# Kernel optimization log

Measured on AMD Instinct MI355X. Metric: run time of the kernel, lower is better.

## Reference

```python
import jax, jax.numpy as jnp
import numpy as np

D_MODEL = 512
N_HEADS = 8
D_K = D_MODEL // N_HEADS


def setup_inputs() -> dict:
    key = jax.random.key(0)
    k1, k2, k3 = jax.random.split(key, 3)
    x = jax.random.normal(k1, (2, 4096, D_MODEL), dtype=jnp.float32)
    # torch Linear weights: [out, in]; we store transposed [in, out] for x @ W
    s_qkv = 1.0 / np.sqrt(D_MODEL)
    W_qkv = jax.random.uniform(k2, (D_MODEL, 3 * D_MODEL), dtype=jnp.float32, minval=-s_qkv, maxval=s_qkv)
    W_out = jax.random.uniform(k3, (D_MODEL, D_MODEL), dtype=jnp.float32, minval=-s_qkv, maxval=s_qkv)
    return {"x": x, "W_qkv": W_qkv, "W_out": W_out}


def reference(x, W_qkv, W_out):
    B, S, _ = x.shape
    qkv = (x @ W_qkv).reshape(B, S, 3, N_HEADS, D_K)
    q, k, v = qkv[:, :, 0], qkv[:, :, 1], qkv[:, :, 2]  # [B,S,H,Dk]
    scale = 1.0 / np.sqrt(D_K).astype(np.float32)
    scores = jnp.einsum('bshd,bthd->bhst', q, k) * scale  # [B,H,S,S]
    attn = jax.nn.softmax(scores, axis=-1)
    out = jnp.einsum('bhst,bthd->bshd', attn, v).reshape(B, S, D_MODEL)
    return out @ W_out
```

## Files before the change

### kernel.cpp

```cpp
#include <hip/hip_runtime.h>
#include <hip/hip_bf16.h>

#define SEQ 4096
#define NB 2
#define DM 512
#define NH 8
#define DK 64

typedef __bf16 bf16;
typedef __bf16 bf16x4 __attribute__((ext_vector_type(4)));
typedef __bf16 bf16x8 __attribute__((ext_vector_type(8)));
typedef float  f32x4 __attribute__((ext_vector_type(4)));

__device__ __forceinline__ f32x4 mfma16(bf16x8 a, bf16x8 b, f32x4 c) {
    return __builtin_amdgcn_mfma_f32_16x16x32_bf16(a, b, c, 0, 0, 0);
}

__device__ __forceinline__ float fexp2(float x) {
    return __builtin_amdgcn_exp2f(x);
}

__device__ __forceinline__ void gload_lds16(const bf16* g, bf16* l) {
    __builtin_amdgcn_global_load_lds(
        (const __attribute__((address_space(1))) void*)g,
        (__attribute__((address_space(3))) void*)l, 16, 0, 0);
}

__device__ __forceinline__ int swzE(int row, int e) {
    return row * 64 + (e ^ ((row & 7) << 3));
}

__device__ __forceinline__ bf16x8 cvt8(const float* __restrict__ p) {
    const float4 v0 = *(const float4*)p;
    const float4 v1 = *(const float4*)(p + 4);
    return (bf16x8){(bf16)v0.x, (bf16)v0.y, (bf16)v0.z, (bf16)v0.w,
                    (bf16)v1.x, (bf16)v1.y, (bf16)v1.z, (bf16)v1.w};
}

__global__ __launch_bounds__(256)
void prep_w2(const float* __restrict__ Wqkv, const float* __restrict__ Wout,
             bf16* __restrict__ Wqh, bf16* __restrict__ Woh) {
    __shared__ float T[64][65];
    const int t = threadIdx.x;
    const int bx = blockIdx.x, by = blockIdx.y;
    const float* W; bf16* D; int N, n0;
    if (by < 24) { W = Wqkv; D = Wqh; N = 3 * DM; n0 = by * 64; }
    else         { W = Wout; D = Woh; N = DM;     n0 = (by - 24) * 64; }
    const int k0 = bx * 64;
    #pragma unroll
    for (int i = 0; i < 4; ++i) {
        int r = i * 16 + (t >> 4);
        int c = (t & 15) * 4;
        float4 v = *(const float4*)&W[(size_t)(k0 + r) * N + n0 + c];
        T[r][c + 0] = v.x; T[r][c + 1] = v.y; T[r][c + 2] = v.z; T[r][c + 3] = v.w;
    }
    __syncthreads();
    #pragma unroll
    for (int i = 0; i < 4; ++i) {
        int n = i * 16 + (t >> 4);
        int c = (t & 15) * 4;
        bf16x4 hv = (bf16x4){(bf16)T[c + 0][n], (bf16)T[c + 1][n],
                             (bf16)T[c + 2][n], (bf16)T[c + 3][n]};
        *(bf16x4*)&D[(size_t)(n0 + n) * DM + k0 + c] = hv;
    }
}

__global__ __launch_bounds__(256, 2)
void gemm_qkv(const float* __restrict__ A, const bf16* __restrict__ Bth,
              bf16* __restrict__ Qout, bf16* __restrict__ Kout,
              bf16* __restrict__ Vout, int M, int N, int K) {
    __shared__ __align__(16) char smem_raw[36864];
    bf16* Ah = (bf16*)smem_raw;
    bf16* Bh = Ah + 128 * 64;

    const int t = threadIdx.x;
    const int lane = t & 63, w = t >> 6;
    const int l15 = lane & 15, g = lane >> 4;
    const int wm = (w >> 1) * 64, wn = (w & 1) * 64;
    const int rowA = blockIdx.y * 128;
    const int colB = blockIdx.x * 128;
    const int sr = t >> 1;
    const int sc = (t & 1) * 32;

    f32x4 acc[4][4] = {};

    for (int k0 = 0; k0 < K; k0 += 64) {
        __syncthreads();
        #pragma unroll
        for (int u = 0; u < 4; ++u) {
            int off = swzE(sr, sc + u * 8);
            *(bf16x8*)&Ah[off] = cvt8(&A[(size_t)(rowA + sr) * K + k0 + sc + u * 8]);
        }
        #pragma unroll
        for (int u = 0; u < 4; ++u) {
            int off = swzE(sr, sc + u * 8);
            *(bf16x8*)&Bh[off] = *(const bf16x8*)&Bth[(size_t)(colB + sr) * K + k0 + sc + u * 8];
        }
        __syncthreads();
        #pragma unroll
        for (int kst = 0; kst < 2; ++kst) {
            bf16x8 ah[4];
            #pragma unroll
            for (int mi = 0; mi < 4; ++mi) {
                int off = swzE(wm + mi * 16 + l15, kst * 32 + g * 8);
                ah[mi] = *(const bf16x8*)&Ah[off];
            }
            #pragma unroll
            for (int ni = 0; ni < 4; ++ni) {
                int off = swzE(wn + ni * 16 + l15, kst * 32 + g * 8);
                bf16x8 bh = *(const bf16x8*)&Bh[off];
                #pragma unroll
                for (int mi = 0; mi < 4; ++mi)
                    acc[mi][ni] = mfma16(ah[mi], bh, acc[mi][ni]);
            }
        }
    }

    const int sec = colB >> 9;
    const float scl = (sec == 0) ? 0.125f * 1.44269504088896f : 1.0f;
    bf16* TB = (bf16*)smem_raw;
    __syncthreads();
    #pragma unroll
    for (int mi = 0; mi < 4; ++mi)
        #pragma unroll
        for (int ni = 0; ni < 4; ++ni)
            #pragma unroll
            for (int r = 0; r < 4; ++r) {
                const int rr = wm + mi * 16 + g * 4 + r;
                const int cr = wn + ni * 16 + l15;
                const float v = acc[mi][ni][r] * scl;
                if (sec < 2) {
                    TB[rr * 136 + cr] = (bf16)v;
                } else {
                    const int kk = rr & 63;
                    const int nn = kk >> 4;
                    const int sl = ((nn & 1) << 5) | (((kk >> 2) & 3) << 3)
                                 | ((nn >> 1) << 2) | (kk & 3);
                    TB[cr * 136 + (rr >> 6) * 64 + sl] = (bf16)v;
                }
            }
    __syncthreads();
    const int b_ = rowA >> 12;
    const int sbase = rowA & 4095;
    #pragma unroll
    for (int pass = 0; pass < 8; ++pass) {
        const int rowi = pass * 16 + (t >> 4);
        const int e8 = (t & 15) * 8;
        bf16x8 v = *(const bf16x8*)&TB[rowi * 136 + e8];
        if (sec < 2) {
            const int ckv = (colB & 511) + e8;
            const int h_ = ckv >> 6, d8 = ckv & 63;
            bf16* dst = (sec == 0) ? Qout : Kout;
            *(bf16x8*)&dst[(((size_t)b_ * NH + h_) * SEQ + sbase + rowi) * DK + d8] = v;
        } else {
            const int cv = (colB - 1024) + rowi;
            const int h_ = cv >> 6, d_ = cv & 63;
            *(bf16x8*)&Vout[(((size_t)b_ * NH + h_) * DK + d_) * SEQ + sbase + e8] = v;
        }
    }
}

__global__ __launch_bounds__(256, 2)
void gemm_out(const bf16* __restrict__ A, const bf16* __restrict__ Bth,
              float* __restrict__ C, int M, int N, int K) {
    __shared__ __align__(16) bf16 Ah[128 * 64], Bh[128 * 64];

    const int t = threadIdx.x;
    const int lane = t & 63, w = t >> 6;
    const int l15 = lane & 15, g = lane >> 4;
    const int wm = (w >> 1) * 64, wn = (w & 1) * 64;
    const int rowA = blockIdx.y * 128;
    const int colB = blockIdx.x * 128;
    const int sr = t >> 1;
    const int sc = (t & 1) * 32;

    f32x4 acc[4][4] = {};

    for (int k0 = 0; k0 < K; k0 += 64) {
        __syncthreads();
        #pragma unroll
        for (int u = 0; u < 4; ++u) {
            int off = swzE(sr, sc + u * 8);
            *(bf16x8*)&Ah[off] = *(const bf16x8*)&A[(size_t)(rowA + sr) * K + k0 + sc + u * 8];
            *(bf16x8*)&Bh[off] = *(const bf16x8*)&Bth[(size_t)(colB + sr) * K + k0 + sc + u * 8];
        }
        __syncthreads();
        #pragma unroll
        for (int kst = 0; kst < 2; ++kst) {
            bf16x8 ah[4];
            #pragma unroll
            for (int mi = 0; mi < 4; ++mi) {
                int off = swzE(wm + mi * 16 + l15, kst * 32 + g * 8);
                ah[mi] = *(const bf16x8*)&Ah[off];
            }
            #pragma unroll
            for (int ni = 0; ni < 4; ++ni) {
                int off = swzE(wn + ni * 16 + l15, kst * 32 + g * 8);
                bf16x8 bh = *(const bf16x8*)&Bh[off];
                #pragma unroll
                for (int mi = 0; mi < 4; ++mi)
                    acc[mi][ni] = mfma16(ah[mi], bh, acc[mi][ni]);
            }
        }
    }
    #pragma unroll
    for (int mi = 0; mi < 4; ++mi)
        #pragma unroll
        for (int ni = 0; ni < 4; ++ni)
            #pragma unroll
            for (int r = 0; r < 4; ++r) {
                int row = rowA + wm + mi * 16 + g * 4 + r;
                int col = colB + wn + ni * 16 + l15;
                C[(size_t)row * N + col] = acc[mi][ni][r];
            }
}

__global__ __launch_bounds__(512)
void flash_mfma(const bf16* __restrict__ Qh,
                const bf16* __restrict__ Kh, const bf16* __restrict__ Vth,
                bf16* __restrict__ att) {
    extern __shared__ bf16 smem[];
    bf16* KhS = smem;
    bf16* VhS = smem + 8192;

    const int nwg = (int)gridDim.x;
    const int cpx = nwg >> 3;
    const int bid = (int)blockIdx.x;
    const int wg = (bid & 7) * cpx + (bid >> 3);
    const int qt = wg & 31;
    const int bh = wg >> 5;

    const int t = threadIdx.x, lane = t & 63, w = t >> 6;
    const int l15 = lane & 15, g = lane >> 4;
    const int q0 = qt * 128;
    const int wq = w * 16;

    bf16x8 qh[2];
    {
        const size_t qbase = ((size_t)bh * SEQ + q0 + wq + l15) * DK + g * 8;
        qh[0] = *(const bf16x8*)&Qh[qbase];
        qh[1] = *(const bf16x8*)&Qh[qbase + 32];
    }

    const bf16 one = (bf16)1.0f;
    const bf16x8 ones = (bf16x8){one, one, one, one, one, one, one, one};

    f32x4 o[4] = {};
    f32x4 lacc = {0.f, 0.f, 0.f, 0.f};

    const int sr = t >> 3;
    const int sc8 = (t & 7) * 8;
    const int scs = sc8 ^ ((sr & 7) << 3);
    const size_t kgo = ((size_t)bh * SEQ + sr) * DK + scs;
    const size_t vgo = ((size_t)bh * DK + sr) * SEQ + scs;
    const int dst = t * 8;

    auto stage = [&](int kt, int c) {
        const int cb = c * 4096 + dst;
        gload_lds16(Kh + kgo + (size_t)kt * 64 * DK, KhS + cb);
        gload_lds16(Vth + vgo + (size_t)kt * 64,     VhS + cb);
    };

    const int NT = SEQ / 64;
    stage(0, 0);
    __syncthreads();

    for (int kt = 0; kt < NT; ++kt) {
        const int c = kt & 1;
        if (kt + 1 < NT) stage(kt + 1, c ^ 1);
        const int cb = c * 4096;

        f32x4 s[4] = {};
        __builtin_amdgcn_s_setprio(1);
        #pragma unroll
        for (int kst = 0; kst < 2; ++kst) {
            #pragma unroll
            for (int ni = 0; ni < 4; ++ni) {
                int off = cb + swzE(ni * 16 + l15, kst * 32 + g * 8);
                bf16x8 kh_ = *(const bf16x8*)&KhS[off];
                s[ni] = mfma16(kh_, qh[kst], s[ni]);
            }
        }
        __builtin_amdgcn_s_setprio(0);

        bf16x8 pa[2];
        #pragma unroll
        for (int ni = 0; ni < 4; ++ni)
            #pragma unroll
            for (int r = 0; r < 4; ++r)
                pa[ni & 1][(ni >> 1) * 4 + r] = (bf16)fexp2(s[ni][r]);

        __builtin_amdgcn_s_setprio(1);
        #pragma unroll
        for (int kst = 0; kst < 2; ++kst) {
            #pragma unroll
            for (int ni = 0; ni < 4; ++ni) {
                int off = cb + swzE(ni * 16 + l15, kst * 32 + g * 8);
                bf16x8 vh_ = *(const bf16x8*)&VhS[off];
                o[ni] = mfma16(pa[kst], vh_, o[ni]);
            }
            lacc = mfma16(pa[kst], ones, lacc);
        }
        __builtin_amdgcn_s_setprio(0);

        __syncthreads();
    }

    const int b = bh >> 3, h = bh & 7;
    #pragma unroll
    for (int r = 0; r < 4; ++r) {
        const float inv = 1.0f / lacc[r];
        const int row = q0 + wq + g * 4 + r;
        #pragma unroll
        for (int ni = 0; ni < 4; ++ni)
            att[(size_t)(b * SEQ + row) * DM + h * DK + ni * 16 + l15] =
                (bf16)(o[ni][r] * inv);
    }
}

extern "C" void kernel_launch(void* const* d_in, const int* in_sizes, int n_in,
                              void* d_out, int out_size, void* d_ws, size_t ws_size,
                              hipStream_t stream) {
    const float* x    = (const float*)d_in[0];
    const float* Wqkv = (const float*)d_in[1];
    const float* Wout = (const float*)d_in[2];
    float* out = (float*)d_out;

    char* ws = (char*)d_ws;
    bf16* Qhp  = (bf16*)(ws);
    bf16* attn = (bf16*)(ws + (size_t)48 * 1048576);
    bf16* Khp  = (bf16*)(ws + (size_t)64 * 1048576);
    bf16* Vthp = (bf16*)(ws + (size_t)80 * 1048576);
    bf16* Wqh  = (bf16*)(ws + (size_t)96 * 1048576);
    bf16* Woh  = (bf16*)(ws + (size_t)100 * 1048576);

    const int M = NB * SEQ;
    const int FLASH_LDS = 32768;

    hipFuncSetAttribute((const void*)flash_mfma,
                        hipFuncAttributeMaxDynamicSharedMemorySize, FLASH_LDS);

    prep_w2<<<dim3(DM / 64, 32), 256, 0, stream>>>(Wqkv, Wout, Wqh, Woh);

    gemm_qkv<<<dim3((3 * DM) / 128, M / 128), 256, 0, stream>>>(
        x, Wqh, Qhp, Khp, Vthp, M, 3 * DM, DM);

    flash_mfma<<<dim3((SEQ / 128) * NH * NB), 512, FLASH_LDS, stream>>>(
        Qhp, Khp, Vthp, attn);

    gemm_out<<<dim3(DM / 128, M / 128), 256, 0, stream>>>(
        attn, Woh, out, M, DM, DM);
}
```

Measured before the change: 132.4 us.

## Pre-convert x to bf16 and stage GEMM tiles via direct global-to-LDS loads

Folds conversion of x from fp32 to bf16 into the weight-prep kernel, so gemm_qkv reads bf16 activations once instead of reconverting fp32 for each of its 12 column blocks. Both GEMMs now fill their shared-memory tiles with global_load_lds 16-byte loads, applying the XOR swizzle on the source address and skipping the VGPR round trip. This adds an extra pass that writes an 8 MB bf16 copy of x to the workspace.

```diff
diff --git a/kernel.cpp b/kernel.cpp
--- a/kernel.cpp
+++ b/kernel.cpp
@@ -38,11 +38,27 @@
 }
 
 __global__ __launch_bounds__(256)
-void prep_w2(const float* __restrict__ Wqkv, const float* __restrict__ Wout,
-             bf16* __restrict__ Wqh, bf16* __restrict__ Woh) {
+void prep_all(const float* __restrict__ Wqkv, const float* __restrict__ Wout,
+              const float* __restrict__ x,
+              bf16* __restrict__ Wqh, bf16* __restrict__ Woh,
+              bf16* __restrict__ xh) {
     __shared__ float T[64][65];
     const int t = threadIdx.x;
     const int bx = blockIdx.x, by = blockIdx.y;
+
+    if (by >= 32) {
+        const int r0 = ((by - 32) * 8 + bx) * 128;
+        #pragma unroll
+        for (int i = 0; i < 32; ++i) {
+            const int idx = i * 256 + t;
+            const int rr = idx >> 6;
+            const int cc = (idx & 63) * 8;
+            const size_t o = (size_t)(r0 + rr) * DM + cc;
+            *(bf16x8*)&xh[o] = cvt8(&x[o]);
+        }
+        return;
+    }
+
     const float* W; bf16* D; int N, n0;
     if (by < 24) { W = Wqkv; D = Wqh; N = 3 * DM; n0 = by * 64; }
     else         { W = Wout; D = Woh; N = DM;     n0 = (by - 24) * 64; }
@@ -66,7 +82,7 @@
 }
 
 __global__ __launch_bounds__(256, 2)
-void gemm_qkv(const float* __restrict__ A, const bf16* __restrict__ Bth,
+void gemm_qkv(const bf16* __restrict__ A, const bf16* __restrict__ Bth,
               bf16* __restrict__ Qout, bf16* __restrict__ Kout,
               bf16* __restrict__ Vout, int M, int N, int K) {
     __shared__ __align__(16) char smem_raw[36864];
@@ -79,22 +95,22 @@
     const int wm = (w >> 1) * 64, wn = (w & 1) * 64;
     const int rowA = blockIdx.y * 128;
     const int colB = blockIdx.x * 128;
-    const int sr = t >> 1;
-    const int sc = (t & 1) * 32;
+
+    const int sr2 = t >> 3;
+    const int sc8 = (t & 7) * 8;
+    const int scs = sc8 ^ ((sr2 & 7) << 3);
+    const int dstE = t * 8;
 
     f32x4 acc[4][4] = {};
 
     for (int k0 = 0; k0 < K; k0 += 64) {
         __syncthreads();
         #pragma unroll
-        for (int u = 0; u < 4; ++u) {
-            int off = swzE(sr, sc + u * 8);
-            *(bf16x8*)&Ah[off] = cvt8(&A[(size_t)(rowA + sr) * K + k0 + sc + u * 8]);
-        }
-        #pragma unroll
-        for (int u = 0; u < 4; ++u) {
-            int off = swzE(sr, sc + u * 8);
-            *(bf16x8*)&Bh[off] = *(const bf16x8*)&Bth[(size_t)(colB + sr) * K + k0 + sc + u * 8];
+        for (int c = 0; c < 4; ++c) {
+            gload_lds16(&A[(size_t)(rowA + c * 32 + sr2) * K + k0 + scs],
+                        Ah + c * 2048 + dstE);
+            gload_lds16(&Bth[(size_t)(colB + c * 32 + sr2) * K + k0 + scs],
+                        Bh + c * 2048 + dstE);
         }
         __syncthreads();
         #pragma unroll
@@ -171,18 +187,22 @@
     const int wm = (w >> 1) * 64, wn = (w & 1) * 64;
     const int rowA = blockIdx.y * 128;
     const int colB = blockIdx.x * 128;
-    const int sr = t >> 1;
-    const int sc = (t & 1) * 32;
+
+    const int sr2 = t >> 3;
+    const int sc8 = (t & 7) * 8;
+    const int scs = sc8 ^ ((sr2 & 7) << 3);
+    const int dstE = t * 8;
 
     f32x4 acc[4][4] = {};
 
     for (int k0 = 0; k0 < K; k0 += 64) {
         __syncthreads();
         #pragma unroll
-        for (int u = 0; u < 4; ++u) {
-            int off = swzE(sr, sc + u * 8);
-            *(bf16x8*)&Ah[off] = *(const bf16x8*)&A[(size_t)(rowA + sr) * K + k0 + sc + u * 8];
-            *(bf16x8*)&Bh[off] = *(const bf16x8*)&Bth[(size_t)(colB + sr) * K + k0 + sc + u * 8];
+        for (int c = 0; c < 4; ++c) {
+            gload_lds16(&A[(size_t)(rowA + c * 32 + sr2) * K + k0 + scs],
+                        Ah + c * 2048 + dstE);
+            gload_lds16(&Bth[(size_t)(colB + c * 32 + sr2) * K + k0 + scs],
+                        Bh + c * 2048 + dstE);
         }
         __syncthreads();
         #pragma unroll
@@ -328,6 +348,7 @@
 
     char* ws = (char*)d_ws;
     bf16* Qhp  = (bf16*)(ws);
+    bf16* xh   = (bf16*)(ws + (size_t)16 * 1048576);
     bf16* attn = (bf16*)(ws + (size_t)48 * 1048576);
     bf16* Khp  = (bf16*)(ws + (size_t)64 * 1048576);
     bf16* Vthp = (bf16*)(ws + (size_t)80 * 1048576);
@@ -340,10 +361,10 @@
     hipFuncSetAttribute((const void*)flash_mfma,
                         hipFuncAttributeMaxDynamicSharedMemorySize, FLASH_LDS);
 
-    prep_w2<<<dim3(DM / 64, 32), 256, 0, stream>>>(Wqkv, Wout, Wqh, Woh);
+    prep_all<<<dim3(8, 40), 256, 0, stream>>>(Wqkv, Wout, x, Wqh, Woh, xh);
 
     gemm_qkv<<<dim3((3 * DM) / 128, M / 128), 256, 0, stream>>>(
-        x, Wqh, Qhp, Khp, Vthp, M, 3 * DM, DM);
+        xh, Wqh, Qhp, Khp, Vthp, M, 3 * DM, DM);
 
     flash_mfma<<<dim3((SEQ / 128) * NH * NB), 512, FLASH_LDS, stream>>>(
         Qhp, Khp, Vthp, attn);
```

Measured after the change: 117.1 us, median of 2. 1.13x faster.
